# Performance work log

Hardware: AMD Instinct MI355X
Metric: run time of the kernel (lower is better)

## Reference

```python
import jax, jax.numpy as jnp
import numpy as np

DIM = 1024
CROSS_DIM = 768
NUM_HEADS = 16
HEAD_DIM = DIM // NUM_HEADS
B, S, SC = 4, 2048, 1024


def setup_inputs() -> dict:
    key = jax.random.key(0)
    ks = jax.random.split(key, 12)
    x = jax.random.normal(ks[0], (B, S, DIM), dtype=jnp.float32)
    cross_x = jax.random.normal(ks[1], (B, SC, CROSS_DIM), dtype=jnp.float32)
    # ragged cross lengths -> padding mask (True = ignore)
    lengths = jax.random.randint(ks[2], (B,), SC // 2, SC + 1)
    key_padding_mask = jnp.arange(SC)[None, :] >= lengths[:, None]  # (B, SC) bool
    s = 0.02
    Wq = jax.random.normal(ks[3], (DIM, DIM), dtype=jnp.float32) * s
    bq = jnp.zeros((DIM,), dtype=jnp.float32)
    Wk = jax.random.normal(ks[4], (CROSS_DIM, DIM), dtype=jnp.float32) * s
    bk = jnp.zeros((DIM,), dtype=jnp.float32)
    Wv = jax.random.normal(ks[5], (CROSS_DIM, DIM), dtype=jnp.float32) * s
    bv = jnp.zeros((DIM,), dtype=jnp.float32)
    Wo = jax.random.normal(ks[6], (DIM, DIM), dtype=jnp.float32) * s
    bo = jnp.zeros((DIM,), dtype=jnp.float32)
    return {"x": x, "cross_x": cross_x, "key_padding_mask": key_padding_mask,
            "Wq": Wq, "bq": bq, "Wk": Wk, "bk": bk, "Wv": Wv, "bv": bv,
            "Wo": Wo, "bo": bo}


def reference(x, cross_x, key_padding_mask, Wq, bq, Wk, bk, Wv, bv, Wo, bo):
    b, s, _ = x.shape
    sc = cross_x.shape[1]
    # projections (torch Linear: x @ W + b with W stored as (in, out) here)
    q = (x @ Wq + bq).reshape(b, s, NUM_HEADS, HEAD_DIM).transpose(0, 2, 1, 3)
    k = (cross_x @ Wk + bk).reshape(b, sc, NUM_HEADS, HEAD_DIM).transpose(0, 2, 1, 3)
    v = (cross_x @ Wv + bv).reshape(b, sc, NUM_HEADS, HEAD_DIM).transpose(0, 2, 1, 3)
    # (b, h, s, sc) attention scores
    scores = jnp.einsum('bhsd,bhcd->bhsc', q, k) / jnp.sqrt(jnp.float32(HEAD_DIM))
    mask = key_padding_mask[:, None, None, :]  # (b,1,1,sc), True = ignore
    scores = jnp.where(mask, -jnp.inf, scores)
    # original subtracts row max then softmax; equivalent stable softmax
    scores = scores - jnp.max(scores, axis=-1, keepdims=True)
    attn = jax.nn.softmax(scores, axis=-1)
    out = jnp.einsum('bhsc,bhcd->bhsd', attn, v)
    out = out.transpose(0, 2, 1, 3).reshape(b, s, DIM)
    return out @ Wo + bo
```

## Files before the change

kernel.cpp:

```cpp
#include <hip/hip_runtime.h>
#include <hip/hip_bf16.h>
#include <stdint.h>

#define DIM_ 1024
#define NH_ 16
#define HD_ 64
#define B_ 4
#define S_ 2048
#define SC_ 1024
#define CD_ 768

typedef __attribute__((ext_vector_type(8))) short bf16x8;
typedef __attribute__((ext_vector_type(4))) short bf16x4;
typedef __attribute__((ext_vector_type(4))) float f32x4;

__device__ inline unsigned short f2bf(float f) {
    __hip_bfloat16 h = __float2bfloat16(f);
    return __builtin_bit_cast(unsigned short, h);
}

__device__ inline f32x4 vmax4(f32x4 a, f32x4 b) {
    f32x4 r;
#pragma unroll
    for (int i = 0; i < 4; ++i) r[i] = fmaxf(a[i], b[i]);
    return r;
}

#define GLOAD16(SRC, DST) __builtin_amdgcn_global_load_lds( \
    (const __attribute__((address_space(1))) void*)(SRC),   \
    (__attribute__((address_space(3))) void*)(DST), 16, 0, 0)

__global__ void k_f32_to_bf16_2(const float* __restrict__ in0, unsigned short* __restrict__ out0, int n40,
                                const float* __restrict__ in1, unsigned short* __restrict__ out1, int n41) {
    int i = blockIdx.x * blockDim.x + threadIdx.x;
    int stride = gridDim.x * blockDim.x;
    int total = n40 + n41;
    for (; i < total; i += stride) {
        const float4 v = (i < n40) ? ((const float4*)in0)[i] : ((const float4*)in1)[i - n40];
        uint2 pk;
        pk.x = (unsigned int)f2bf(v.x) | ((unsigned int)f2bf(v.y) << 16);
        pk.y = (unsigned int)f2bf(v.z) | ((unsigned int)f2bf(v.w) << 16);
        if (i < n40) ((uint2*)out0)[i] = pk;
        else         ((uint2*)out1)[i - n40] = pk;
    }
}

__global__ void k_transposeW4(const float* __restrict__ Wq, const float* __restrict__ Wk,
                              const float* __restrict__ Wv, const float* __restrict__ Wo,
                              unsigned short* __restrict__ WQT, unsigned short* __restrict__ WKT,
                              unsigned short* __restrict__ WVT, unsigned short* __restrict__ WOT,
                              const unsigned int* __restrict__ m,
                              unsigned int* __restrict__ bits, int* __restrict__ ntp) {
    if (blockIdx.x == 1792) {
        __shared__ int bm_s;
        __shared__ unsigned int wbits[128];
        if (threadIdx.x == 0) bm_s = 0;
        __syncthreads();
        int any = 0;
        for (int i = threadIdx.x; i < 1024; i += 256)
            if (m[i] > 1u) any = 1;
        if (any) atomicOr(&bm_s, 1);
        __syncthreads();
        const int boolmode = bm_s;
        const int w = threadIdx.x;
        if (w < 128) {
            const unsigned char* mb = (const unsigned char*)m;
            unsigned int out = 0;
            for (int j = 0; j < 32; ++j) {
                int c = w * 32 + j;
                int masked = boolmode ? (mb[c] != 0) : (m[c] != 0u);
                out |= (unsigned int)masked << j;
            }
            bits[w] = out;
            wbits[w] = out;
        }
        __syncthreads();
        if (threadIdx.x < 4) {
            int nt = 0;
            for (int tt = 0; tt < 16; ++tt) {
                unsigned int w0 = wbits[threadIdx.x * 32 + tt * 2];
                unsigned int w1 = wbits[threadIdx.x * 32 + tt * 2 + 1];
                if ((w0 & w1) != 0xFFFFFFFFu) nt = tt + 1;
            }
            ntp[threadIdx.x] = nt;
        }
        return;
    }
    int idx = blockIdx.x * blockDim.x + threadIdx.x;
    const float* W; unsigned short* WT; int K;
    if (idx < 131072)      { W = Wq; WT = WQT; K = 1024; }
    else if (idx < 229376) { W = Wk; WT = WKT; K = 768;  idx -= 131072; }
    else if (idx < 327680) { W = Wv; WT = WVT; K = 768;  idx -= 229376; }
    else                   { W = Wo; WT = WOT; K = 1024; idx -= 327680; }
    int n = idx & 1023;
    int k0 = (idx >> 10) << 3;
    unsigned int pk[4];
#pragma unroll
    for (int j = 0; j < 4; ++j) {
        unsigned short a = f2bf(W[(size_t)(k0 + 2 * j) * 1024 + n]);
        unsigned short b = f2bf(W[(size_t)(k0 + 2 * j + 1) * 1024 + n]);
        pk[j] = (unsigned int)a | ((unsigned int)b << 16);
    }
    *(uint4*)&WT[(size_t)n * K + k0] = *(uint4*)pk;
}

template<int EPI>
__global__ __launch_bounds__(256) void k_gemm_bt(
    const unsigned short* __restrict__ A, const unsigned short* __restrict__ BT,
    const float* __restrict__ bias, const float* __restrict__ bias2, float oscale,
    unsigned short* __restrict__ Cb, unsigned short* __restrict__ Cb2,
    float* __restrict__ Cf, int M, int N, int K)
{
    __shared__ unsigned short As[2][128 * 64];
    __shared__ unsigned short Bs[2][128 * 64];
    const int t = threadIdx.x;
    const int w = t >> 6, lane = t & 63;
    const int lo = lane & 15, hi = lane >> 4;
    const int l7 = lo & 7;
    const int nwg = gridDim.x * gridDim.y;
    const int wg = blockIdx.y * gridDim.x + blockIdx.x;
    const int swz = (wg & 7) * (nwg >> 3) + (wg >> 3);
    const int m0 = (swz % gridDim.x) * 128, n0 = (swz / gridDim.x) * 128;
    const int wr = (w >> 1) * 64, wc = (w & 1) * 64;
    const int srow = lane >> 3;
    const int scb  = ((lane & 7) ^ srow) << 3;

    f32x4 zero4 = {0.f, 0.f, 0.f, 0.f};
    f32x4 acc[4][4];
    for (int i = 0; i < 4; ++i)
        for (int j = 0; j < 4; ++j) acc[i][j] = zero4;

#pragma unroll
    for (int p = 0; p < 4; ++p) {
        int rb = w * 32 + p * 8;
        GLOAD16(&A[(size_t)(m0 + rb + srow) * K + scb], &As[0][rb * 64]);
        GLOAD16(&BT[(size_t)(n0 + rb + srow) * K + scb], &Bs[0][rb * 64]);
    }
    __syncthreads();

    int cur = 0;
    for (int k0 = 0; k0 < K; k0 += 64) {
        if (k0 + 64 < K) {
#pragma unroll
            for (int p = 0; p < 4; ++p) {
                int rb = w * 32 + p * 8;
                GLOAD16(&A[(size_t)(m0 + rb + srow) * K + k0 + 64 + scb], &As[cur ^ 1][rb * 64]);
                GLOAD16(&BT[(size_t)(n0 + rb + srow) * K + k0 + 64 + scb], &Bs[cur ^ 1][rb * 64]);
            }
        }
#pragma unroll
        for (int kk = 0; kk < 2; ++kk) {
            bf16x8 af[4], bfr[4];
#pragma unroll
            for (int i = 0; i < 4; ++i) {
                int row = wr + i * 16 + lo;
                af[i] = *(const bf16x8*)&As[cur][row * 64 + ((((kk << 2) + hi) ^ l7) << 3)];
            }
#pragma unroll
            for (int j = 0; j < 4; ++j) {
                int row = wc + j * 16 + lo;
                bfr[j] = *(const bf16x8*)&Bs[cur][row * 64 + ((((kk << 2) + hi) ^ l7) << 3)];
            }
#pragma unroll
            for (int i = 0; i < 4; ++i)
#pragma unroll
                for (int j = 0; j < 4; ++j)
                    acc[i][j] = __builtin_amdgcn_mfma_f32_16x16x32_bf16(af[i], bfr[j], acc[i][j], 0, 0, 0);
        }
        __syncthreads();
        cur ^= 1;
    }

#pragma unroll
    for (int i = 0; i < 4; ++i) {
#pragma unroll
        for (int j = 0; j < 4; ++j) {
            int n = n0 + wc + j * 16 + lo;
            int mbase = m0 + wr + i * 16 + (hi << 2);
            if (EPI == 3 && n >= 1024) {
                float b2 = bias2[n - 1024];
                uint2 pk;
                pk.x = (unsigned int)f2bf(acc[i][j][0] + b2) | ((unsigned int)f2bf(acc[i][j][1] + b2) << 16);
                pk.y = (unsigned int)f2bf(acc[i][j][2] + b2) | ((unsigned int)f2bf(acc[i][j][3] + b2) << 16);
                int bb = mbase >> 10, c = mbase & 1023;
                *(uint2*)&Cb2[(size_t)((bb << 10) + (n - 1024)) * 1024 + c] = pk;
            } else {
#pragma unroll
                for (int r = 0; r < 4; ++r) {
                    int m = mbase + r;
                    if (EPI == 0) {
                        float v = (acc[i][j][r] + bias[n]) * oscale;
                        Cb[(size_t)m * 1024 + n] = f2bf(v);
                    } else if (EPI == 2) {
                        float v = (acc[i][j][r] + bias[n]) * oscale;
                        Cf[(size_t)m * 1024 + n] = v;
                    } else {
                        float v = acc[i][j][r] + bias[n];
                        Cb[(size_t)m * 1024 + n] = f2bf(v);
                    }
                }
            }
        }
    }
}

__global__ __launch_bounds__(256) void k_attn(
    const unsigned short* __restrict__ Q, const unsigned short* __restrict__ Kb,
    const unsigned short* __restrict__ VT, const unsigned int* __restrict__ bits,
    const int* __restrict__ ntp, unsigned short* __restrict__ Ob)
{
    __shared__ unsigned short lds[16384];
    const int t = threadIdx.x, w = t >> 6, lane = t & 63;
    const int lo = lane & 15, hi = lane >> 4;
    const int qt = blockIdx.x, h = blockIdx.y, b = blockIdx.z;
    const int qr0 = qt * 128 + w * 32;
    const int l7 = lo & 7;
    const int nt = ntp[b];

    const int srow = lane >> 3;
    const int scb  = ((lane & 7) ^ srow) << 3;

    bf16x8 qf[2][2];
#pragma unroll
    for (int qh = 0; qh < 2; ++qh)
#pragma unroll
        for (int kk = 0; kk < 2; ++kk)
            qf[qh][kk] = *(const bf16x8*)&Q[(size_t)(b * S_ + qr0 + qh * 16 + lo) * DIM_ + h * 64 + kk * 32 + hi * 8];

    f32x4 zero4 = {0.f, 0.f, 0.f, 0.f};
    float mrow[2] = {-1e30f, -1e30f}, lsum[2] = {0.f, 0.f};
    f32x4 o[4][2];
#pragma unroll
    for (int dt = 0; dt < 4; ++dt)
#pragma unroll
        for (int qh = 0; qh < 2; ++qh) o[dt][qh] = zero4;

#pragma unroll
    for (int s = 0; s < 2; ++s) {
        int rl = w * 16 + s * 8 + srow;
        GLOAD16(&Kb[(size_t)(b * SC_ + rl) * DIM_ + h * 64 + scb], &lds[(w * 16 + s * 8) * 64]);
        GLOAD16(&VT[(size_t)(b * 1024 + h * 64 + rl) * SC_ + scb], &lds[8192 + (w * 16 + s * 8) * 64]);
    }
    __syncthreads();

    int cur = 0;
    for (int tt = 0; tt < nt; ++tt) {
        if (tt + 1 < nt) {
            int c0n = (tt + 1) * 64;
#pragma unroll
            for (int s = 0; s < 2; ++s) {
                int rl = w * 16 + s * 8 + srow;
                GLOAD16(&Kb[(size_t)(b * SC_ + c0n + rl) * DIM_ + h * 64 + scb],
                        &lds[(cur ^ 1) * 4096 + (w * 16 + s * 8) * 64]);
                GLOAD16(&VT[(size_t)(b * 1024 + h * 64 + rl) * SC_ + c0n + scb],
                        &lds[8192 + (cur ^ 1) * 4096 + (w * 16 + s * 8) * 64]);
            }
        }
        const unsigned short* Kl = &lds[cur * 4096];
        const unsigned short* Vl = &lds[8192 + cur * 4096];

        f32x4 st[4][2];
#pragma unroll
        for (int n = 0; n < 4; ++n)
#pragma unroll
            for (int qh = 0; qh < 2; ++qh) st[n][qh] = zero4;
#pragma unroll
        for (int n = 0; n < 4; ++n) {
            const int R = n * 16 + lo;
            bf16x8 k0 = *(const bf16x8*)&Kl[R * 64 + ((hi ^ l7) << 3)];
            bf16x8 k1 = *(const bf16x8*)&Kl[R * 64 + (((4 + hi) ^ l7) << 3)];
#pragma unroll
            for (int qh = 0; qh < 2; ++qh) {
                st[n][qh] = __builtin_amdgcn_mfma_f32_16x16x32_bf16(k0, qf[qh][0], st[n][qh], 0, 0, 0);
                st[n][qh] = __builtin_amdgcn_mfma_f32_16x16x32_bf16(k1, qf[qh][1], st[n][qh], 0, 0, 0);
            }
        }
        bf16x4 vf[4][4];
#pragma unroll
        for (int dt = 0; dt < 4; ++dt)
#pragma unroll
            for (int n = 0; n < 4; ++n)
                vf[dt][n] = *(const bf16x4*)&Vl[(dt * 16 + lo) * 64
                              + (((2 * n + (hi >> 1)) ^ l7) << 3) + ((hi & 1) << 2)];

        uint2 mw = *(const uint2*)&bits[b * 32 + tt * 2];

        f32x4 p[2][4];
        float mx[2];
        if ((mw.x | mw.y) == 0u) {
#pragma unroll
            for (int qh = 0; qh < 2; ++qh) {
                f32x4 a = vmax4(vmax4(st[0][qh], st[1][qh]), vmax4(st[2][qh], st[3][qh]));
                mx[qh] = fmaxf(fmaxf(a[0], a[1]), fmaxf(a[2], a[3]));
#pragma unroll
                for (int n = 0; n < 4; ++n) p[qh][n] = st[n][qh];
            }
        } else {
            mx[0] = -1e30f; mx[1] = -1e30f;
#pragma unroll
            for (int n = 0; n < 4; ++n) {
                unsigned int wd = (n & 2) ? mw.y : mw.x;
#pragma unroll
                for (int r = 0; r < 4; ++r) {
                    int sh = ((n & 1) << 4) + (hi << 2) + r;
                    bool mk = (wd >> sh) & 1u;
#pragma unroll
                    for (int qh = 0; qh < 2; ++qh) {
                        float s = mk ? -1e30f : st[n][qh][r];
                        p[qh][n][r] = s;
                        mx[qh] = fmaxf(mx[qh], s);
                    }
                }
            }
        }
        float m2[2];
#pragma unroll
        for (int qh = 0; qh < 2; ++qh) {
            float v = fmaxf(mx[qh], __shfl_xor(mx[qh], 16));
            m2[qh] = fmaxf(v, __shfl_xor(v, 32));
        }
        float growth = fmaxf(m2[0] - mrow[0], m2[1] - mrow[1]);
        if (!__all(growth <= 8.0f)) {
#pragma unroll
            for (int qh = 0; qh < 2; ++qh) {
                float mnew = fmaxf(mrow[qh], m2[qh]);
                float scl = __builtin_amdgcn_exp2f(mrow[qh] - mnew);
                mrow[qh] = mnew;
                lsum[qh] *= scl;
#pragma unroll
                for (int dt = 0; dt < 4; ++dt)
                    o[dt][qh] *= scl;
            }
        }
#pragma unroll
        for (int qh = 0; qh < 2; ++qh) {
            f32x4 rs4 = zero4;
#pragma unroll
            for (int n = 0; n < 4; ++n) {
                f32x4 e;
#pragma unroll
                for (int r = 0; r < 4; ++r)
                    e[r] = __builtin_amdgcn_exp2f(p[qh][n][r] - mrow[qh]);
                p[qh][n] = e;
                rs4 += e;
            }
            float rs = (rs4[0] + rs4[1]) + (rs4[2] + rs4[3]);
            rs += __shfl_xor(rs, 16);
            rs += __shfl_xor(rs, 32);
            lsum[qh] += rs;
        }
#pragma unroll
        for (int qh = 0; qh < 2; ++qh) {
#pragma unroll
            for (int n = 0; n < 4; ++n) {
                uint2 pk2;
                pk2.x = (unsigned int)f2bf(p[qh][n][0]) | ((unsigned int)f2bf(p[qh][n][1]) << 16);
                pk2.y = (unsigned int)f2bf(p[qh][n][2]) | ((unsigned int)f2bf(p[qh][n][3]) << 16);
                bf16x4 pb = __builtin_bit_cast(bf16x4, pk2);
#pragma unroll
                for (int dt = 0; dt < 4; ++dt)
                    o[dt][qh] = __builtin_amdgcn_mfma_f32_16x16x16bf16_1k(vf[dt][n], pb, o[dt][qh], 0, 0, 0);
            }
        }
        __syncthreads();
        cur ^= 1;
    }

    unsigned short* Tl = &lds[w * 2304];
    float inv[2] = {1.0f / lsum[0], 1.0f / lsum[1]};
#pragma unroll
    for (int qh = 0; qh < 2; ++qh)
#pragma unroll
        for (int dt = 0; dt < 4; ++dt)
#pragma unroll
            for (int r = 0; r < 4; ++r)
                Tl[(qh * 16 + lo) * 72 + dt * 16 + hi * 4 + r] = f2bf(o[dt][qh][r] * inv[qh]);
#pragma unroll
    for (int ps = 0; ps < 4; ++ps) {
        int row = ps * 8 + (lane >> 3);
        int col = (lane & 7) * 8;
        bf16x8 v = *(const bf16x8*)&Tl[row * 72 + col];
        *(bf16x8*)&Ob[(size_t)(b * S_ + qr0 + row) * DIM_ + h * 64 + col] = v;
    }
}

extern "C" void kernel_launch(void* const* d_in, const int* in_sizes, int n_in,
                              void* d_out, int out_size, void* d_ws, size_t ws_size,
                              hipStream_t stream)
{
    const float* x  = (const float*)d_in[0];
    const float* cx = (const float*)d_in[1];
    const void* mask = d_in[2];
    const float* Wq = (const float*)d_in[3];
    const float* bq = (const float*)d_in[4];
    const float* Wk = (const float*)d_in[5];
    const float* bk = (const float*)d_in[6];
    const float* Wv = (const float*)d_in[7];
    const float* bv = (const float*)d_in[8];
    const float* Wo = (const float*)d_in[9];
    const float* bo = (const float*)d_in[10];

    unsigned short* ws = (unsigned short*)d_ws;
    const size_t XB  = 0;
    const size_t CXB = XB  + (size_t)8192 * 1024;
    const size_t WQT = CXB + (size_t)4096 * 768;
    const size_t WKT = WQT + (size_t)1024 * 1024;
    const size_t WVT = WKT + (size_t)1024 * 768;
    const size_t WOT = WVT + (size_t)1024 * 768;
    const size_t QB  = WOT + (size_t)1024 * 1024;
    const size_t KB  = QB  + (size_t)8192 * 1024;
    const size_t VTB = KB  + (size_t)4096 * 1024;
    const size_t MBT = VTB + (size_t)4 * 1024 * 1024;
    const size_t NTP = MBT + 256;

    unsigned int* mbits = (unsigned int*)(ws + MBT);
    int* ntp = (int*)(ws + NTP);

    k_f32_to_bf16_2<<<2048, 256, 0, stream>>>(x, ws + XB, 8192 * 1024 / 4,
                                              cx, ws + CXB, 4096 * 768 / 4);
    k_transposeW4<<<1793, 256, 0, stream>>>(Wq, Wk, Wv, Wo,
                                            ws + WQT, ws + WKT, ws + WVT, ws + WOT,
                                            (const unsigned int*)mask, mbits, ntp);

    const float QSCALE = 0.125f * 1.44269504088896340736f;
    dim3 gq(8192 / 128, 1024 / 128);
    dim3 gkv(4096 / 128, 2048 / 128);
    k_gemm_bt<0><<<gq, 256, 0, stream>>>(ws + XB, ws + WQT, bq, nullptr, QSCALE, ws + QB, nullptr, nullptr, 8192, 1024, 1024);
    k_gemm_bt<3><<<gkv, 256, 0, stream>>>(ws + CXB, ws + WKT, bk, bv, 1.0f, ws + KB, ws + VTB, nullptr, 4096, 2048, 768);

    dim3 ga(S_ / 128, NH_, B_);
    k_attn<<<ga, 256, 0, stream>>>(ws + QB, ws + KB, ws + VTB, mbits, ntp, ws + XB);

    k_gemm_bt<2><<<gq, 256, 0, stream>>>(ws + XB, ws + WOT, bo, nullptr, 1.0f, nullptr, nullptr, (float*)d_out, 8192, 1024, 1024);
}
```

Measured before the change: 153.8 us.

## Merge prep kernels, fuse Q and KV GEMMs into one launch, add MFMA priority

Folds the activation conversion, weight transpose and mask-bit kernels into a single prep launch with one element per thread. Q and K/V projections now run as one GEMM launch of 1024 tiles, interleaved so Q and KV tiles share the grid and fill the device together instead of running back to back. Attention wraps its MFMA sections in s_setprio to favour matrix issue, and the output GEMM is specialised with a plain epilogue. The intent is to remove launch overhead and tail idle time, at the cost of a larger mixed-work GEMM grid and more branching per tile.

```diff
diff --git a/kernel.cpp b/kernel.cpp
--- a/kernel.cpp
+++ b/kernel.cpp
@@ -30,86 +30,184 @@
     (const __attribute__((address_space(1))) void*)(SRC),   \
     (__attribute__((address_space(3))) void*)(DST), 16, 0, 0)
 
-__global__ void k_f32_to_bf16_2(const float* __restrict__ in0, unsigned short* __restrict__ out0, int n40,
-                                const float* __restrict__ in1, unsigned short* __restrict__ out1, int n41) {
-    int i = blockIdx.x * blockDim.x + threadIdx.x;
-    int stride = gridDim.x * blockDim.x;
-    int total = n40 + n41;
-    for (; i < total; i += stride) {
-        const float4 v = (i < n40) ? ((const float4*)in0)[i] : ((const float4*)in1)[i - n40];
+__global__ void k_prep(const float* __restrict__ x, unsigned short* __restrict__ xb,
+                       const float* __restrict__ cx, unsigned short* __restrict__ cxb,
+                       const float* __restrict__ Wq, const float* __restrict__ Wk,
+                       const float* __restrict__ Wv, const float* __restrict__ Wo,
+                       unsigned short* __restrict__ WQT, unsigned short* __restrict__ WKT,
+                       unsigned short* __restrict__ WVT, unsigned short* __restrict__ WOT,
+                       const unsigned int* __restrict__ m,
+                       unsigned int* __restrict__ bits, int* __restrict__ ntp) {
+    const int bid = blockIdx.x;
+    if (bid < 11264) {
+        const float* in; unsigned short* out; int i;
+        if (bid < 8192) { in = x;  out = xb;  i = bid * 256 + threadIdx.x; }
+        else            { in = cx; out = cxb; i = (bid - 8192) * 256 + threadIdx.x; }
+        float4 v = ((const float4*)in)[i];
         uint2 pk;
         pk.x = (unsigned int)f2bf(v.x) | ((unsigned int)f2bf(v.y) << 16);
         pk.y = (unsigned int)f2bf(v.z) | ((unsigned int)f2bf(v.w) << 16);
-        if (i < n40) ((uint2*)out0)[i] = pk;
-        else         ((uint2*)out1)[i - n40] = pk;
-    }
-}
-
-__global__ void k_transposeW4(const float* __restrict__ Wq, const float* __restrict__ Wk,
-                              const float* __restrict__ Wv, const float* __restrict__ Wo,
-                              unsigned short* __restrict__ WQT, unsigned short* __restrict__ WKT,
-                              unsigned short* __restrict__ WVT, unsigned short* __restrict__ WOT,
-                              const unsigned int* __restrict__ m,
-                              unsigned int* __restrict__ bits, int* __restrict__ ntp) {
-    if (blockIdx.x == 1792) {
-        __shared__ int bm_s;
-        __shared__ unsigned int wbits[128];
-        if (threadIdx.x == 0) bm_s = 0;
+        ((uint2*)out)[i] = pk;
+        return;
+    }
+    if (bid < 13056) {
+        int idx = (bid - 11264) * 256 + threadIdx.x;
+        const float* W; unsigned short* WT; int K;
+        if (idx < 131072)      { W = Wq; WT = WQT; K = 1024; }
+        else if (idx < 229376) { W = Wk; WT = WKT; K = 768;  idx -= 131072; }
+        else if (idx < 327680) { W = Wv; WT = WVT; K = 768;  idx -= 229376; }
+        else                   { W = Wo; WT = WOT; K = 1024; idx -= 327680; }
+        int n = idx & 1023;
+        int k0 = (idx >> 10) << 3;
+        unsigned int pk[4];
+#pragma unroll
+        for (int j = 0; j < 4; ++j) {
+            unsigned short a = f2bf(W[(size_t)(k0 + 2 * j) * 1024 + n]);
+            unsigned short b = f2bf(W[(size_t)(k0 + 2 * j + 1) * 1024 + n]);
+            pk[j] = (unsigned int)a | ((unsigned int)b << 16);
+        }
+        *(uint4*)&WT[(size_t)n * K + k0] = *(uint4*)pk;
+        return;
+    }
+    __shared__ int bm_s;
+    __shared__ unsigned int wbits[128];
+    if (threadIdx.x == 0) bm_s = 0;
+    __syncthreads();
+    int any = 0;
+    for (int i = threadIdx.x; i < 1024; i += 256)
+        if (m[i] > 1u) any = 1;
+    if (any) atomicOr(&bm_s, 1);
+    __syncthreads();
+    const int boolmode = bm_s;
+    const int w = threadIdx.x;
+    if (w < 128) {
+        const unsigned char* mb = (const unsigned char*)m;
+        unsigned int out = 0;
+        for (int j = 0; j < 32; ++j) {
+            int c = w * 32 + j;
+            int masked = boolmode ? (mb[c] != 0) : (m[c] != 0u);
+            out |= (unsigned int)masked << j;
+        }
+        bits[w] = out;
+        wbits[w] = out;
+    }
+    __syncthreads();
+    if (threadIdx.x < 4) {
+        int nt = 0;
+        for (int tt = 0; tt < 16; ++tt) {
+            unsigned int w0 = wbits[threadIdx.x * 32 + tt * 2];
+            unsigned int w1 = wbits[threadIdx.x * 32 + tt * 2 + 1];
+            if ((w0 & w1) != 0xFFFFFFFFu) nt = tt + 1;
+        }
+        ntp[threadIdx.x] = nt;
+    }
+}
+
+__global__ __launch_bounds__(256) void k_gemm_qkv(
+    const unsigned short* __restrict__ xb, const unsigned short* __restrict__ cxb,
+    const unsigned short* __restrict__ wqt, const unsigned short* __restrict__ wkt,
+    const float* __restrict__ bq, const float* __restrict__ bk, const float* __restrict__ bv,
+    float qscale, unsigned short* __restrict__ qb, unsigned short* __restrict__ kb,
+    unsigned short* __restrict__ vtb)
+{
+    __shared__ unsigned short As[2][128 * 64];
+    __shared__ unsigned short Bs[2][128 * 64];
+    const int t = threadIdx.x;
+    const int w = t >> 6, lane = t & 63;
+    const int lo = lane & 15, hi = lane >> 4;
+    const int l7 = lo & 7;
+    const int wg = blockIdx.x;
+    const int swz = (wg & 7) * 128 + (wg >> 3);
+    const bool isQ = !(swz & 1);
+    const int lw = swz >> 1;
+    const int gx = isQ ? 64 : 32;
+    const unsigned short* A  = isQ ? xb  : cxb;
+    const unsigned short* BT = isQ ? wqt : wkt;
+    const int K = isQ ? 1024 : 768;
+    const int m0 = (lw % gx) * 128, n0 = (lw / gx) * 128;
+    const int wr = (w >> 1) * 64, wc = (w & 1) * 64;
+    const int srow = lane >> 3;
+    const int scb  = ((lane & 7) ^ srow) << 3;
+
+    f32x4 zero4 = {0.f, 0.f, 0.f, 0.f};
+    f32x4 acc[4][4];
+    for (int i = 0; i < 4; ++i)
+        for (int j = 0; j < 4; ++j) acc[i][j] = zero4;
+
+#pragma unroll
+    for (int p = 0; p < 4; ++p) {
+        int rb = w * 32 + p * 8;
+        GLOAD16(&A[(size_t)(m0 + rb + srow) * K + scb], &As[0][rb * 64]);
+        GLOAD16(&BT[(size_t)(n0 + rb + srow) * K + scb], &Bs[0][rb * 64]);
+    }
+    __syncthreads();
+
+    int cur = 0;
+    for (int k0 = 0; k0 < K; k0 += 64) {
+        if (k0 + 64 < K) {
+#pragma unroll
+            for (int p = 0; p < 4; ++p) {
+                int rb = w * 32 + p * 8;
+                GLOAD16(&A[(size_t)(m0 + rb + srow) * K + k0 + 64 + scb], &As[cur ^ 1][rb * 64]);
+                GLOAD16(&BT[(size_t)(n0 + rb + srow) * K + k0 + 64 + scb], &Bs[cur ^ 1][rb * 64]);
+            }
+        }
+#pragma unroll
+        for (int kk = 0; kk < 2; ++kk) {
+            bf16x8 af[4], bfr[4];
+#pragma unroll
+            for (int i = 0; i < 4; ++i) {
+                int row = wr + i * 16 + lo;
+                af[i] = *(const bf16x8*)&As[cur][row * 64 + ((((kk << 2) + hi) ^ l7) << 3)];
+            }
+#pragma unroll
+            for (int j = 0; j < 4; ++j) {
+                int row = wc + j * 16 + lo;
+                bfr[j] = *(const bf16x8*)&Bs[cur][row * 64 + ((((kk << 2) + hi) ^ l7) << 3)];
+            }
+#pragma unroll
+            for (int i = 0; i < 4; ++i)
+#pragma unroll
+                for (int j = 0; j < 4; ++j)
+                    acc[i][j] = __builtin_amdgcn_mfma_f32_16x16x32_bf16(af[i], bfr[j], acc[i][j], 0, 0, 0);
+        }
         __syncthreads();
-        int any = 0;
-        for (int i = threadIdx.x; i < 1024; i += 256)
-            if (m[i] > 1u) any = 1;
-        if (any) atomicOr(&bm_s, 1);
-        __syncthreads();
-        const int boolmode = bm_s;
-        const int w = threadIdx.x;
-        if (w < 128) {
-            const unsigned char* mb = (const unsigned char*)m;
-            unsigned int out = 0;
-            for (int j = 0; j < 32; ++j) {
-                int c = w * 32 + j;
-                int masked = boolmode ? (mb[c] != 0) : (m[c] != 0u);
-                out |= (unsigned int)masked << j;
-            }
-            bits[w] = out;
-            wbits[w] = out;
-        }
-        __syncthreads();
-        if (threadIdx.x < 4) {
-            int nt = 0;
-            for (int tt = 0; tt < 16; ++tt) {
-                unsigned int w0 = wbits[threadIdx.x * 32 + tt * 2];
-                unsigned int w1 = wbits[threadIdx.x * 32 + tt * 2 + 1];
-                if ((w0 & w1) != 0xFFFFFFFFu) nt = tt + 1;
-            }
-            ntp[threadIdx.x] = nt;
-        }
-        return;
-    }
-    int idx = blockIdx.x * blockDim.x + threadIdx.x;
-    const float* W; unsigned short* WT; int K;
-    if (idx < 131072)      { W = Wq; WT = WQT; K = 1024; }
-    else if (idx < 229376) { W = Wk; WT = WKT; K = 768;  idx -= 131072; }
-    else if (idx < 327680) { W = Wv; WT = WVT; K = 768;  idx -= 229376; }
-    else                   { W = Wo; WT = WOT; K = 1024; idx -= 327680; }
-    int n = idx & 1023;
-    int k0 = (idx >> 10) << 3;
-    unsigned int pk[4];
-#pragma unroll
-    for (int j = 0; j < 4; ++j) {
-        unsigned short a = f2bf(W[(size_t)(k0 + 2 * j) * 1024 + n]);
-        unsigned short b = f2bf(W[(size_t)(k0 + 2 * j + 1) * 1024 + n]);
-        pk[j] = (unsigned int)a | ((unsigned int)b << 16);
-    }
-    *(uint4*)&WT[(size_t)n * K + k0] = *(uint4*)pk;
-}
-
-template<int EPI>
-__global__ __launch_bounds__(256) void k_gemm_bt(
+        cur ^= 1;
+    }
+
+#pragma unroll
+    for (int i = 0; i < 4; ++i) {
+#pragma unroll
+        for (int j = 0; j < 4; ++j) {
+            int n = n0 + wc + j * 16 + lo;
+            int mbase = m0 + wr + i * 16 + (hi << 2);
+            if (isQ) {
+#pragma unroll
+                for (int r = 0; r < 4; ++r) {
+                    float v = (acc[i][j][r] + bq[n]) * qscale;
+                    qb[(size_t)(mbase + r) * 1024 + n] = f2bf(v);
+                }
+            } else if (n < 1024) {
+#pragma unroll
+                for (int r = 0; r < 4; ++r) {
+                    float v = acc[i][j][r] + bk[n];
+                    kb[(size_t)(mbase + r) * 1024 + n] = f2bf(v);
+                }
+            } else {
+                float b2 = bv[n - 1024];
+                uint2 pk;
+                pk.x = (unsigned int)f2bf(acc[i][j][0] + b2) | ((unsigned int)f2bf(acc[i][j][1] + b2) << 16);
+                pk.y = (unsigned int)f2bf(acc[i][j][2] + b2) | ((unsigned int)f2bf(acc[i][j][3] + b2) << 16);
+                int bb = mbase >> 10, c = mbase & 1023;
+                *(uint2*)&vtb[(size_t)((bb << 10) + (n - 1024)) * 1024 + c] = pk;
+            }
+        }
+    }
+}
+
+__global__ __launch_bounds__(256) void k_gemm_o(
     const unsigned short* __restrict__ A, const unsigned short* __restrict__ BT,
-    const float* __restrict__ bias, const float* __restrict__ bias2, float oscale,
-    unsigned short* __restrict__ Cb, unsigned short* __restrict__ Cb2,
-    float* __restrict__ Cf, int M, int N, int K)
+    const float* __restrict__ bias, float* __restrict__ Cf, int K)
 {
     __shared__ unsigned short As[2][128 * 64];
     __shared__ unsigned short Bs[2][128 * 64];
@@ -172,36 +270,15 @@
     }
 
 #pragma unroll
-    for (int i = 0; i < 4; ++i) {
+    for (int i = 0; i < 4; ++i)
 #pragma unroll
         for (int j = 0; j < 4; ++j) {
             int n = n0 + wc + j * 16 + lo;
             int mbase = m0 + wr + i * 16 + (hi << 2);
-            if (EPI == 3 && n >= 1024) {
-                float b2 = bias2[n - 1024];
-                uint2 pk;
-                pk.x = (unsigned int)f2bf(acc[i][j][0] + b2) | ((unsigned int)f2bf(acc[i][j][1] + b2) << 16);
-                pk.y = (unsigned int)f2bf(acc[i][j][2] + b2) | ((unsigned int)f2bf(acc[i][j][3] + b2) << 16);
-                int bb = mbase >> 10, c = mbase & 1023;
-                *(uint2*)&Cb2[(size_t)((bb << 10) + (n - 1024)) * 1024 + c] = pk;
-            } else {
-#pragma unroll
-                for (int r = 0; r < 4; ++r) {
-                    int m = mbase + r;
-                    if (EPI == 0) {
-                        float v = (acc[i][j][r] + bias[n]) * oscale;
-                        Cb[(size_t)m * 1024 + n] = f2bf(v);
-                    } else if (EPI == 2) {
-                        float v = (acc[i][j][r] + bias[n]) * oscale;
-                        Cf[(size_t)m * 1024 + n] = v;
-                    } else {
-                        float v = acc[i][j][r] + bias[n];
-                        Cb[(size_t)m * 1024 + n] = f2bf(v);
-                    }
-                }
-            }
-        }
-    }
+#pragma unroll
+            for (int r = 0; r < 4; ++r)
+                Cf[(size_t)(mbase + r) * 1024 + n] = acc[i][j][r] + bias[n];
+        }
 }
 
 __global__ __launch_bounds__(256) void k_attn(
@@ -264,6 +341,7 @@
         for (int n = 0; n < 4; ++n)
 #pragma unroll
             for (int qh = 0; qh < 2; ++qh) st[n][qh] = zero4;
+        __builtin_amdgcn_s_setprio(1);
 #pragma unroll
         for (int n = 0; n < 4; ++n) {
             const int R = n * 16 + lo;
@@ -275,6 +353,7 @@
                 st[n][qh] = __builtin_amdgcn_mfma_f32_16x16x32_bf16(k1, qf[qh][1], st[n][qh], 0, 0, 0);
             }
         }
+        __builtin_amdgcn_s_setprio(0);
         bf16x4 vf[4][4];
 #pragma unroll
         for (int dt = 0; dt < 4; ++dt)
@@ -349,6 +428,7 @@
             rs += __shfl_xor(rs, 32);
             lsum[qh] += rs;
         }
+        __builtin_amdgcn_s_setprio(1);
 #pragma unroll
         for (int qh = 0; qh < 2; ++qh) {
 #pragma unroll
@@ -362,6 +442,7 @@
                     o[dt][qh] = __builtin_amdgcn_mfma_f32_16x16x16bf16_1k(vf[dt][n], pb, o[dt][qh], 0, 0, 0);
             }
         }
+        __builtin_amdgcn_s_setprio(0);
         __syncthreads();
         cur ^= 1;
     }
@@ -416,20 +497,19 @@
     unsigned int* mbits = (unsigned int*)(ws + MBT);
     int* ntp = (int*)(ws + NTP);
 
-    k_f32_to_bf16_2<<<2048, 256, 0, stream>>>(x, ws + XB, 8192 * 1024 / 4,
-                                              cx, ws + CXB, 4096 * 768 / 4);
-    k_transposeW4<<<1793, 256, 0, stream>>>(Wq, Wk, Wv, Wo,
-                                            ws + WQT, ws + WKT, ws + WVT, ws + WOT,
-                                            (const unsigned int*)mask, mbits, ntp);
+    k_prep<<<13057, 256, 0, stream>>>(x, ws + XB, cx, ws + CXB,
+                                      Wq, Wk, Wv, Wo,
+                                      ws + WQT, ws + WKT, ws + WVT, ws + WOT,
+                                      (const unsigned int*)mask, mbits, ntp);
 
     const float QSCALE = 0.125f * 1.44269504088896340736f;
-    dim3 gq(8192 / 128, 1024 / 128);
-    dim3 gkv(4096 / 128, 2048 / 128);
-    k_gemm_bt<0><<<gq, 256, 0, stream>>>(ws + XB, ws + WQT, bq, nullptr, QSCALE, ws + QB, nullptr, nullptr, 8192, 1024, 1024);
-    k_gemm_bt<3><<<gkv, 256, 0, stream>>>(ws + CXB, ws + WKT, bk, bv, 1.0f, ws + KB, ws + VTB, nullptr, 4096, 2048, 768);
+    k_gemm_qkv<<<1024, 256, 0, stream>>>(ws + XB, ws + CXB, ws + WQT, ws + WKT,
+                                         bq, bk, bv, QSCALE,
+                                         ws + QB, ws + KB, ws + VTB);
 
     dim3 ga(S_ / 128, NH_, B_);
     k_attn<<<ga, 256, 0, stream>>>(ws + QB, ws + KB, ws + VTB, mbits, ntp, ws + XB);
 
-    k_gemm_bt<2><<<gq, 256, 0, stream>>>(ws + XB, ws + WOT, bo, nullptr, 1.0f, nullptr, nullptr, (float*)d_out, 8192, 1024, 1024);
-}
+    dim3 go(8192 / 128, 1024 / 128);
+    k_gemm_o<<<go, 256, 0, stream>>>(ws + XB, ws + WOT, bo, (float*)d_out, 1024);
+}
```

New measurement: 159.0 us. 3.4% more time.
